# Optimization experiments

Measured on AMD Instinct MI355X. Metric: run time of the kernel, lower is better.

The kernel has to match this reference:

```python
import jax, jax.numpy as jnp
import numpy as np

N_VARS = 4000
N_LITS = 2 * N_VARS
N_CLAUSES = 16000
N_CELLS = 48000
DIM = 128
N_ROUNDS = 16
N_PROBS = 8


def _mlp(x, w1, b1, w2, b2, w3, b3):
    x = jax.nn.relu(x @ w1.T + b1)
    x = jax.nn.relu(x @ w2.T + b2)
    return x @ w3.T + b3


def _lstm_step(x, h, c, wih, whh, bih, bhh):
    # PyTorch LSTM gate order: i, f, g, o
    gates = x @ wih.T + bih + h @ whh.T + bhh
    i, f, g, o = jnp.split(gates, 4, axis=-1)
    c = jax.nn.sigmoid(f) * c + jax.nn.sigmoid(i) * jnp.tanh(g)
    h = jax.nn.sigmoid(o) * jnp.tanh(c)
    return h, c


def setup_inputs() -> dict:
    key = jax.random.key(0)
    ks = iter(jax.random.split(key, 64))

    def p(shape, scale=0.05):
        return jax.random.normal(next(ks), shape, dtype=jnp.float32) * scale

    lit_idx = jax.random.randint(next(ks), (N_CELLS,), 0, N_LITS)
    cls_idx = jax.random.randint(next(ks), (N_CELLS,), 0, N_CLAUSES)
    L_unpack_indices = jnp.stack([lit_idx, cls_idx], axis=1)  # [n_cells, 2]

    return dict(
        L_unpack_indices=L_unpack_indices,
        n_vars=N_VARS, n_probs=N_PROBS, n_rounds=N_ROUNDS,
        L_init_w=p((DIM, 1)), L_init_b=p((DIM,)),
        C_init_w=p((DIM, 1)), C_init_b=p((DIM,)),
        Lmsg_w1=p((DIM, DIM)), Lmsg_b1=p((DIM,)),
        Lmsg_w2=p((DIM, DIM)), Lmsg_b2=p((DIM,)),
        Lmsg_w3=p((DIM, DIM)), Lmsg_b3=p((DIM,)),
        Cmsg_w1=p((DIM, DIM)), Cmsg_b1=p((DIM,)),
        Cmsg_w2=p((DIM, DIM)), Cmsg_b2=p((DIM,)),
        Cmsg_w3=p((DIM, DIM)), Cmsg_b3=p((DIM,)),
        Lvote_w1=p((DIM, DIM)), Lvote_b1=p((DIM,)),
        Lvote_w2=p((DIM, DIM)), Lvote_b2=p((DIM,)),
        Lvote_w3=p((1, DIM)), Lvote_b3=p((1,)),
        Lu_wih=p((4 * DIM, 2 * DIM)), Lu_whh=p((4 * DIM, DIM)),
        Lu_bih=p((4 * DIM,)), Lu_bhh=p((4 * DIM,)),
        Cu_wih=p((4 * DIM, DIM)), Cu_whh=p((4 * DIM, DIM)),
        Cu_bih=p((4 * DIM,)), Cu_bhh=p((4 * DIM,)),
    )


def reference(L_unpack_indices, n_vars, n_probs, n_rounds,
              L_init_w, L_init_b, C_init_w, C_init_b,
              Lmsg_w1, Lmsg_b1, Lmsg_w2, Lmsg_b2, Lmsg_w3, Lmsg_b3,
              Cmsg_w1, Cmsg_b1, Cmsg_w2, Cmsg_b2, Cmsg_w3, Cmsg_b3,
              Lvote_w1, Lvote_b1, Lvote_w2, Lvote_b2, Lvote_w3, Lvote_b3,
              Lu_wih, Lu_whh, Lu_bih, Lu_bhh,
              Cu_wih, Cu_whh, Cu_bih, Cu_bhh):
    n_lits = 2 * n_vars
    dim = L_init_b.shape[0]
    n_clauses = N_CLAUSES

    # densified literal-clause incidence matrix (matches torch.sparse -> to_dense)
    M = jnp.zeros((n_lits, n_clauses), jnp.float32).at[
        L_unpack_indices[:, 0], L_unpack_indices[:, 1]].add(1.0)

    # L_init/C_init applied to ts = ones(1)
    L0 = jnp.broadcast_to(L_init_w[:, 0] + L_init_b, (n_lits, dim))
    C0 = jnp.broadcast_to(C_init_w[:, 0] + C_init_b, (n_clauses, dim))
    carry0 = (L0, jnp.zeros((n_lits, dim), jnp.float32),
              C0, jnp.zeros((n_clauses, dim), jnp.float32))

    def round_fn(carry, _):
        Lh, Lc, Ch, Cc = carry
        L_pre = _mlp(Lh, Lmsg_w1, Lmsg_b1, Lmsg_w2, Lmsg_b2, Lmsg_w3, Lmsg_b3)
        LC_msg = M.T @ L_pre                      # [n_clauses, dim]
        Ch, Cc = _lstm_step(LC_msg, Ch, Cc, Cu_wih, Cu_whh, Cu_bih, Cu_bhh)
        C_pre = _mlp(Ch, Cmsg_w1, Cmsg_b1, Cmsg_w2, Cmsg_b2, Cmsg_w3, Cmsg_b3)
        CL_msg = M @ C_pre                        # [n_lits, dim]
        flipped = jnp.concatenate([Lh[n_vars:2 * n_vars], Lh[:n_vars]], axis=0)
        Lh, Lc = _lstm_step(jnp.concatenate([CL_msg, flipped], axis=1),
                            Lh, Lc, Lu_wih, Lu_whh, Lu_bih, Lu_bhh)
        return (Lh, Lc, Ch, Cc), None

    (Lh, _, _, _), _ = jax.lax.scan(round_fn, carry0, None, length=n_rounds)

    vote = _mlp(Lh, Lvote_w1, Lvote_b1, Lvote_w2, Lvote_b2, Lvote_w3, Lvote_b3)  # [n_lits, 1]
    vote_join = jnp.concatenate([vote[:n_vars], vote[n_vars:]], axis=1)          # [n_vars, 2]
    vote_join = vote_join.reshape(n_probs, -1)
    return jnp.mean(vote_join, axis=1)
```

## Files before the change

### kernel.cpp

```cpp
#include <hip/hip_runtime.h>
#include <cstdint>
#include <cstddef>

#define N_VARS   4000
#define N_LITS   8000
#define N_CLAUSES 16000
#define N_CELLS  48000
#define DIM      128
#define N_ROUNDS 16
#define N_PROBS  8

typedef __bf16 bf16x8 __attribute__((ext_vector_type(8)));
typedef float f32x4 __attribute__((ext_vector_type(4)));

__device__ inline unsigned short f2bf(float x) {
  unsigned int u = __float_as_uint(x);
  u += 0x7fffu + ((u >> 16) & 1u);
  return (unsigned short)(u >> 16);
}
__device__ inline float bflo(unsigned int v) { return __uint_as_float(v << 16); }
__device__ inline float bfhi(unsigned int v) { return __uint_as_float(v & 0xffff0000u); }
__device__ inline unsigned int pack2(float a, float b) {
  return (unsigned int)f2bf(a) | ((unsigned int)f2bf(b) << 16);
}
__device__ inline bf16x8 ld_frag(const unsigned short* p) {
  uint4 u = *reinterpret_cast<const uint4*>(p);
  return __builtin_bit_cast(bf16x8, u);
}
__device__ inline float fast_sigmoid(float x) { return 1.f / (1.f + __expf(-x)); }
__device__ inline float fast_tanh(float x) {
  float t = __expf(-2.f * x);
  return (1.f - t) / (1.f + t);
}


template<int KS, bool LIT>
__global__ __launch_bounds__(512, 4) void fused_round(
    const int* __restrict__ ptr, const int* __restrict__ col,
    const unsigned short* __restrict__ Tsrc,
    const unsigned short* hold, unsigned short* hnew,
    float* __restrict__ cst,
    const unsigned short* __restrict__ Wp, const float* __restrict__ bP,
    const unsigned short* __restrict__ Wm1, const float* __restrict__ bm1,
    const unsigned short* __restrict__ Wm2, const float* __restrict__ bm2,
    const unsigned short* __restrict__ Wm3, const float* __restrict__ bm3,
    unsigned short* __restrict__ Tout) {
  __shared__ __align__(16) unsigned short msg[32][136];
  __shared__ __align__(16) unsigned short hsA[32][136];
  __shared__ __align__(16) unsigned short hsF[LIT ? 32 : 1][136];
  __shared__ __align__(16) unsigned short xb[32][136];
  const int tid = threadIdx.x;
  const int w = tid >> 6, l = tid & 63;
  const int r = l & 15, kc = l >> 4;
  const int row0 = blockIdx.x * 32;
  const int flipoff = LIT ? ((row0 < N_VARS) ? N_VARS : -N_VARS) : 0;

  float s[16];
  {
    const int g8 = tid >> 3, gl = tid & 7;
    const int grow = g8 & 31, part = g8 >> 5;
    const int row = row0 + grow;
    const int b = ptr[row], e = ptr[row + 1];
#pragma unroll
    for (int q = 0; q < 16; ++q) s[q] = 0.f;
    int j = b + part;
    int c0 = (j < e) ? col[j] : 0;
    while (j < e) {
      const int jn = j + 2;
      const int c1 = (jn < e) ? col[jn] : 0;
      const unsigned short* src = &Tsrc[(size_t)c0 * 128 + gl * 16];
      const uint4 v0 = *reinterpret_cast<const uint4*>(src);
      const uint4 v1 = *reinterpret_cast<const uint4*>(src + 8);
      s[0]  += bflo(v0.x); s[1]  += bfhi(v0.x);
      s[2]  += bflo(v0.y); s[3]  += bfhi(v0.y);
      s[4]  += bflo(v0.z); s[5]  += bfhi(v0.z);
      s[6]  += bflo(v0.w); s[7]  += bfhi(v0.w);
      s[8]  += bflo(v1.x); s[9]  += bfhi(v1.x);
      s[10] += bflo(v1.y); s[11] += bfhi(v1.y);
      s[12] += bflo(v1.z); s[13] += bfhi(v1.z);
      s[14] += bflo(v1.w); s[15] += bfhi(v1.w);
      j = jn; c0 = c1;
    }
    if (part == 1) {
      uint4 o0, o1;
      o0.x = pack2(s[0], s[1]);  o0.y = pack2(s[2], s[3]);
      o0.z = pack2(s[4], s[5]);  o0.w = pack2(s[6], s[7]);
      o1.x = pack2(s[8], s[9]);  o1.y = pack2(s[10], s[11]);
      o1.z = pack2(s[12], s[13]); o1.w = pack2(s[14], s[15]);
      *reinterpret_cast<uint4*>(&msg[grow][gl * 16]) = o0;
      *reinterpret_cast<uint4*>(&msg[grow][gl * 16 + 8]) = o1;
    }
  }
  __syncthreads();

  {
    const int g8 = tid >> 3, gl = tid & 7;
    const int grow = g8 & 31, part = g8 >> 5;
    if (part == 0) {
      const uint4 m0 = *reinterpret_cast<const uint4*>(&msg[grow][gl * 16]);
      const uint4 m1 = *reinterpret_cast<const uint4*>(&msg[grow][gl * 16 + 8]);
      s[0]  += bflo(m0.x); s[1]  += bfhi(m0.x);
      s[2]  += bflo(m0.y); s[3]  += bfhi(m0.y);
      s[4]  += bflo(m0.z); s[5]  += bfhi(m0.z);
      s[6]  += bflo(m0.w); s[7]  += bfhi(m0.w);
      s[8]  += bflo(m1.x); s[9]  += bfhi(m1.x);
      s[10] += bflo(m1.y); s[11] += bfhi(m1.y);
      s[12] += bflo(m1.z); s[13] += bfhi(m1.z);
      s[14] += bflo(m1.w); s[15] += bfhi(m1.w);
      uint4 o0, o1;
      o0.x = pack2(s[0], s[1]);  o0.y = pack2(s[2], s[3]);
      o0.z = pack2(s[4], s[5]);  o0.w = pack2(s[6], s[7]);
      o1.x = pack2(s[8], s[9]);  o1.y = pack2(s[10], s[11]);
      o1.z = pack2(s[12], s[13]); o1.w = pack2(s[14], s[15]);
      *reinterpret_cast<uint4*>(&msg[grow][gl * 16]) = o0;
      *reinterpret_cast<uint4*>(&msg[grow][gl * 16 + 8]) = o1;
    } else {
      const int sidx = tid - 256;
#pragma unroll
      for (int q = 0; q < 2; ++q) {
        const int n = sidx + q * 256;
        const int rw = n >> 4, c8 = (n & 15) * 8;
        *reinterpret_cast<uint4*>(&hsA[rw][c8]) =
            *reinterpret_cast<const uint4*>(&hold[(size_t)(row0 + rw) * 128 + c8]);
        if (LIT)
          *reinterpret_cast<uint4*>(&hsF[rw][c8]) =
              *reinterpret_cast<const uint4*>(&hold[(size_t)(row0 + flipoff + rw) * 128 + c8]);
      }
    }
  }
  __syncthreads();

  f32x4 acc[2][4];
#pragma unroll
  for (int rg = 0; rg < 2; ++rg)
#pragma unroll
    for (int t = 0; t < 4; ++t) acc[rg][t] = (f32x4){0.f, 0.f, 0.f, 0.f};

#pragma unroll
  for (int ks = 0; ks < KS; ++ks) {
    bf16x8 bfr[2];
#pragma unroll
    for (int rg = 0; rg < 2; ++rg) {
      const int xr = rg * 16 + r;
      if (ks < 4)        bfr[rg] = ld_frag(&msg[xr][ks * 32 + kc * 8]);
      else if (!LIT)     bfr[rg] = ld_frag(&hsA[xr][(ks - 4) * 32 + kc * 8]);
      else if (ks < 8)   bfr[rg] = ld_frag(&hsF[xr][(ks - 4) * 32 + kc * 8]);
      else               bfr[rg] = ld_frag(&hsA[xr][(ks - 8) * 32 + kc * 8]);
    }
#pragma unroll
    for (int tt = 0; tt < 4; ++tt) {
      bf16x8 afr = ld_frag(&Wp[(size_t)(((w * KS + ks) * 4 + tt) * 64 + l) * 8]);
      acc[0][tt] = __builtin_amdgcn_mfma_f32_16x16x32_bf16(afr, bfr[0], acc[0][tt], 0, 0, 0);
      acc[1][tt] = __builtin_amdgcn_mfma_f32_16x16x32_bf16(afr, bfr[1], acc[1][tt], 0, 0, 0);
    }
  }
  __syncthreads();

  {
    const int d0 = w * 16 + kc * 4;
#pragma unroll
    for (int rg = 0; rg < 2; ++rg) {
      const int row = row0 + rg * 16 + r;
      const size_t cb = (size_t)row * 128 + d0;
      f32x4 cv = *reinterpret_cast<const f32x4*>(&cst[cb]);
      f32x4 cn4;
      unsigned int hp[2];
#pragma unroll
      for (int tt = 0; tt < 4; ++tt) {
        const float4 bb = *reinterpret_cast<const float4*>(&bP[w * 64 + tt * 16 + kc * 4]);
        float ig = acc[rg][tt][0] + bb.x;
        float fg = acc[rg][tt][1] + bb.y;
        float gg = acc[rg][tt][2] + bb.z;
        float og = acc[rg][tt][3] + bb.w;
        float cn = fast_sigmoid(fg) * cv[tt] + fast_sigmoid(ig) * fast_tanh(gg);
        float hv = fast_sigmoid(og) * fast_tanh(cn);
        cn4[tt] = cn;
        if (tt & 1) hp[tt >> 1] |= (unsigned int)f2bf(hv) << 16;
        else        hp[tt >> 1]  = (unsigned int)f2bf(hv);
      }
      *reinterpret_cast<f32x4*>(&cst[cb]) = cn4;
      uint2 hv2 = {hp[0], hp[1]};
      *reinterpret_cast<uint2*>(&hnew[cb]) = hv2;
      *reinterpret_cast<uint2*>(&hsA[rg * 16 + r][d0]) = hv2;
    }
  }
  __syncthreads();

  const int mrg = w >> 2;
  const int t0 = (w & 3) * 2;
  {
    f32x4 a2[2] = {(f32x4){0.f, 0.f, 0.f, 0.f}, (f32x4){0.f, 0.f, 0.f, 0.f}};
#pragma unroll
    for (int ks = 0; ks < 4; ++ks) {
      bf16x8 af = ld_frag(&hsA[mrg * 16 + r][ks * 32 + kc * 8]);
#pragma unroll
      for (int q = 0; q < 2; ++q) {
        bf16x8 bf = ld_frag(&Wm1[(size_t)(((t0 + q) * 4 + ks) * 64 + l) * 8]);
        a2[q] = __builtin_amdgcn_mfma_f32_16x16x32_bf16(af, bf, a2[q], 0, 0, 0);
      }
    }
#pragma unroll
    for (int q = 0; q < 2; ++q) {
      float bv = bm1[(t0 + q) * 16 + r];
#pragma unroll
      for (int j = 0; j < 4; ++j)
        xb[mrg * 16 + kc * 4 + j][(t0 + q) * 16 + r] = f2bf(fmaxf(a2[q][j] + bv, 0.f));
    }
  }
  __syncthreads();
  {
    f32x4 a2[2] = {(f32x4){0.f, 0.f, 0.f, 0.f}, (f32x4){0.f, 0.f, 0.f, 0.f}};
#pragma unroll
    for (int ks = 0; ks < 4; ++ks) {
      bf16x8 af = ld_frag(&xb[mrg * 16 + r][ks * 32 + kc * 8]);
#pragma unroll
      for (int q = 0; q < 2; ++q) {
        bf16x8 bf = ld_frag(&Wm2[(size_t)(((t0 + q) * 4 + ks) * 64 + l) * 8]);
        a2[q] = __builtin_amdgcn_mfma_f32_16x16x32_bf16(af, bf, a2[q], 0, 0, 0);
      }
    }
#pragma unroll
    for (int q = 0; q < 2; ++q) {
      float bv = bm2[(t0 + q) * 16 + r];
#pragma unroll
      for (int j = 0; j < 4; ++j)
        msg[mrg * 16 + kc * 4 + j][(t0 + q) * 16 + r] = f2bf(fmaxf(a2[q][j] + bv, 0.f));
    }
  }
  __syncthreads();
  {
    f32x4 a2[2] = {(f32x4){0.f, 0.f, 0.f, 0.f}, (f32x4){0.f, 0.f, 0.f, 0.f}};
#pragma unroll
    for (int ks = 0; ks < 4; ++ks) {
      bf16x8 af = ld_frag(&msg[mrg * 16 + r][ks * 32 + kc * 8]);
#pragma unroll
      for (int q = 0; q < 2; ++q) {
        bf16x8 bf = ld_frag(&Wm3[(size_t)(((t0 + q) * 4 + ks) * 64 + l) * 8]);
        a2[q] = __builtin_amdgcn_mfma_f32_16x16x32_bf16(af, bf, a2[q], 0, 0, 0);
      }
    }
#pragma unroll
    for (int q = 0; q < 2; ++q) {
      float bv = bm3[(t0 + q) * 16 + r];
#pragma unroll
      for (int j = 0; j < 4; ++j)
        Tout[(size_t)(row0 + mrg * 16 + kc * 4 + j) * 128 + (t0 + q) * 16 + r] =
            f2bf(a2[q][j] + bv);
    }
  }
}

__global__ __launch_bounds__(256) void fused_mlp3(
    const unsigned short* __restrict__ A,
    const unsigned short* __restrict__ W1, const float* __restrict__ b1,
    const unsigned short* __restrict__ W2, const float* __restrict__ b2,
    const unsigned short* __restrict__ W3, const float* __restrict__ b3,
    unsigned short* __restrict__ out) {
  __shared__ __align__(16) unsigned short xbuf[2][4][16][136];
  const int w = threadIdx.x >> 6, l = threadIdx.x & 63;
  const int r = l & 15, kc = l >> 4;
  const int row0 = blockIdx.x * 64 + w * 16;

  f32x4 acc[8];
#pragma unroll
  for (int t = 0; t < 8; ++t) acc[t] = (f32x4){0.f, 0.f, 0.f, 0.f};
#pragma unroll
  for (int ks = 0; ks < 4; ++ks) {
    bf16x8 a = ld_frag(&A[(size_t)(row0 + r) * 128 + ks * 32 + kc * 8]);
#pragma unroll
    for (int t = 0; t < 8; ++t) {
      bf16x8 b = ld_frag(&W1[(size_t)((t * 4 + ks) * 64 + l) * 8]);
      acc[t] = __builtin_amdgcn_mfma_f32_16x16x32_bf16(a, b, acc[t], 0, 0, 0);
    }
  }
#pragma unroll
  for (int t = 0; t < 8; ++t) {
    float bv = b1[t * 16 + r];
#pragma unroll
    for (int j = 0; j < 4; ++j)
      xbuf[0][w][kc * 4 + j][t * 16 + r] = f2bf(fmaxf(acc[t][j] + bv, 0.f));
  }
#pragma unroll
  for (int t = 0; t < 8; ++t) acc[t] = (f32x4){0.f, 0.f, 0.f, 0.f};
#pragma unroll
  for (int ks = 0; ks < 4; ++ks) {
    bf16x8 a = ld_frag(&xbuf[0][w][r][ks * 32 + kc * 8]);
#pragma unroll
    for (int t = 0; t < 8; ++t) {
      bf16x8 b = ld_frag(&W2[(size_t)((t * 4 + ks) * 64 + l) * 8]);
      acc[t] = __builtin_amdgcn_mfma_f32_16x16x32_bf16(a, b, acc[t], 0, 0, 0);
    }
  }
#pragma unroll
  for (int t = 0; t < 8; ++t) {
    float bv = b2[t * 16 + r];
#pragma unroll
    for (int j = 0; j < 4; ++j)
      xbuf[1][w][kc * 4 + j][t * 16 + r] = f2bf(fmaxf(acc[t][j] + bv, 0.f));
  }
#pragma unroll
  for (int t = 0; t < 8; ++t) acc[t] = (f32x4){0.f, 0.f, 0.f, 0.f};
#pragma unroll
  for (int ks = 0; ks < 4; ++ks) {
    bf16x8 a = ld_frag(&xbuf[1][w][r][ks * 32 + kc * 8]);
#pragma unroll
    for (int t = 0; t < 8; ++t) {
      bf16x8 b = ld_frag(&W3[(size_t)((t * 4 + ks) * 64 + l) * 8]);
      acc[t] = __builtin_amdgcn_mfma_f32_16x16x32_bf16(a, b, acc[t], 0, 0, 0);
    }
  }
#pragma unroll
  for (int t = 0; t < 8; ++t) {
    float bv = b3[t * 16 + r];
#pragma unroll
    for (int j = 0; j < 4; ++j)
      out[(size_t)(row0 + kc * 4 + j) * 128 + t * 16 + r] = f2bf(acc[t][j] + bv);
  }
}

__global__ __launch_bounds__(256) void fused_vote(
    const unsigned short* __restrict__ A,
    const unsigned short* __restrict__ W1, const float* __restrict__ b1,
    const unsigned short* __restrict__ W2, const float* __restrict__ b2,
    const float* __restrict__ w3, const float* __restrict__ b3,
    float* __restrict__ vote) {
  __shared__ __align__(16) unsigned short xbuf[4][16][136];
  const int w = threadIdx.x >> 6, l = threadIdx.x & 63;
  const int r = l & 15, kc = l >> 4;
  const int row0 = blockIdx.x * 64 + w * 16;

  f32x4 acc[8];
#pragma unroll
  for (int t = 0; t < 8; ++t) acc[t] = (f32x4){0.f, 0.f, 0.f, 0.f};
#pragma unroll
  for (int ks = 0; ks < 4; ++ks) {
    bf16x8 a = ld_frag(&A[(size_t)(row0 + r) * 128 + ks * 32 + kc * 8]);
#pragma unroll
    for (int t = 0; t < 8; ++t) {
      bf16x8 b = ld_frag(&W1[(size_t)((t * 4 + ks) * 64 + l) * 8]);
      acc[t] = __builtin_amdgcn_mfma_f32_16x16x32_bf16(a, b, acc[t], 0, 0, 0);
    }
  }
#pragma unroll
  for (int t = 0; t < 8; ++t) {
    float bv = b1[t * 16 + r];
#pragma unroll
    for (int j = 0; j < 4; ++j)
      xbuf[w][kc * 4 + j][t * 16 + r] = f2bf(fmaxf(acc[t][j] + bv, 0.f));
  }
#pragma unroll
  for (int t = 0; t < 8; ++t) acc[t] = (f32x4){0.f, 0.f, 0.f, 0.f};
#pragma unroll
  for (int ks = 0; ks < 4; ++ks) {
    bf16x8 a = ld_frag(&xbuf[w][r][ks * 32 + kc * 8]);
#pragma unroll
    for (int t = 0; t < 8; ++t) {
      bf16x8 b = ld_frag(&W2[(size_t)((t * 4 + ks) * 64 + l) * 8]);
      acc[t] = __builtin_amdgcn_mfma_f32_16x16x32_bf16(a, b, acc[t], 0, 0, 0);
    }
  }
  float vs[4] = {0.f, 0.f, 0.f, 0.f};
#pragma unroll
  for (int t = 0; t < 8; ++t) {
    float bv = b2[t * 16 + r], wv = w3[t * 16 + r];
#pragma unroll
    for (int j = 0; j < 4; ++j)
      vs[j] += fmaxf(acc[t][j] + bv, 0.f) * wv;
  }
#pragma unroll
  for (int off = 1; off < 16; off <<= 1) {
#pragma unroll
    for (int j = 0; j < 4; ++j) vs[j] += __shfl_xor(vs[j], off, 16);
  }
  if (r == 0) {
#pragma unroll
    for (int j = 0; j < 4; ++j) vote[row0 + kc * 4 + j] = vs[j] + b3[0];
  }
}

__global__ void init_state_kernel(const float* __restrict__ Lw, const float* __restrict__ Lb,
                                  const float* __restrict__ Cw, const float* __restrict__ Cb,
                                  unsigned short* __restrict__ Lh, float* __restrict__ Lc,
                                  unsigned short* __restrict__ Ch, float* __restrict__ Cc) {
  int idx = blockIdx.x * 256 + threadIdx.x;
  if (idx >= N_CLAUSES * DIM) return;
  int d = idx & 127;
  Ch[idx] = f2bf(Cw[d] + Cb[d]);
  Cc[idx] = 0.f;
  if (idx < N_LITS * DIM) {
    Lh[idx] = f2bf(Lw[d] + Lb[d]);
    Lc[idx] = 0.f;
  }
}

__global__ void pack8_kernel(const float* s0, const float* s1, const float* s2, const float* s3,
                             const float* s4, const float* s5, const float* s6, const float* s7,
                             unsigned short* d0, unsigned short* d1, unsigned short* d2,
                             unsigned short* d3, unsigned short* d4, unsigned short* d5,
                             unsigned short* d6, unsigned short* d7) {
  int i = blockIdx.x * 256 + threadIdx.x;
  const float* s; unsigned short* d;
  switch (blockIdx.y) {
    case 0: s = s0; d = d0; break;
    case 1: s = s1; d = d1; break;
    case 2: s = s2; d = d2; break;
    case 3: s = s3; d = d3; break;
    case 4: s = s4; d = d4; break;
    case 5: s = s5; d = d5; break;
    case 6: s = s6; d = d6; break;
    default: s = s7; d = d7; break;
  }
  int np = i >> 7, k = i & 127;
  int tt = np >> 4, r = np & 15;
  int ks = k >> 5, kcf = (k >> 3) & 3, e = k & 7;
  int dst = (((tt * 4 + ks) * 64) + kcf * 16 + r) * 8 + e;
  d[dst] = f2bf(s[i]);
}

template<int KIH>
__global__ void pack_gates_kernel(const float* __restrict__ wih, const float* __restrict__ whh,
                                  const float* __restrict__ bih, const float* __restrict__ bhh,
                                  unsigned short* __restrict__ Wp, float* __restrict__ bP) {
  constexpr int K = KIH + 128;
  constexpr int KS = K / 32;
  int idx = blockIdx.x * 256 + threadIdx.x;
  if (idx >= 512 * K) return;
  int np = idx / K, k = idx % K;
  int gt = np & 3;
  int d = ((np >> 6) << 4) + (((np >> 2) & 3) << 2) + ((np >> 4) & 3);
  int orig = gt * 128 + d;
  float v = (k < KIH) ? wih[(size_t)orig * KIH + k] : whh[(size_t)orig * 128 + (k - KIH)];
  int w = np >> 6, tt = (np >> 4) & 3, r = np & 15;
  int ks = k >> 5, kcf = (k >> 3) & 3, e = k & 7;
  size_t dst = ((size_t)((w * KS + ks) * 4 + tt) * 64 + kcf * 16 + r) * 8 + e;
  Wp[dst] = f2bf(v);
  if (k == 0) bP[np] = bih[orig] + bhh[orig];
}

__global__ void count_kernel(const int* __restrict__ uidx,
                             int* __restrict__ lit_cnt, int* __restrict__ cls_cnt) {
  int i = blockIdx.x * 256 + threadIdx.x;
  if (i < N_CELLS) {
    atomicAdd(&lit_cnt[uidx[2 * i]], 1);
    atomicAdd(&cls_cnt[uidx[2 * i + 1]], 1);
  }
}

__global__ void scan_kernel(const int* __restrict__ cnt, int* __restrict__ ptr, int n) {
  __shared__ int part[1024];
  __shared__ int total;
  int t = threadIdx.x;
  int chunk = (n + 1023) >> 10;
  int lo = t * chunk, hi = min(lo + chunk, n);
  int s = 0;
  for (int i = lo; i < hi; ++i) s += cnt[i];
  part[t] = s;
  __syncthreads();
  if (t == 0) {
    int acc = 0;
    for (int i = 0; i < 1024; ++i) { int v = part[i]; part[i] = acc; acc += v; }
    total = acc;
  }
  __syncthreads();
  int acc = part[t];
  for (int i = lo; i < hi; ++i) { ptr[i] = acc; acc += cnt[i]; }
  if (t == 0) ptr[n] = total;
}

__global__ void scatter_kernel(const int* __restrict__ uidx,
                               const int* __restrict__ lit_ptr, const int* __restrict__ cls_ptr,
                               int* __restrict__ lit_fill, int* __restrict__ cls_fill,
                               int* __restrict__ lit_col, int* __restrict__ cls_col) {
  int i = blockIdx.x * 256 + threadIdx.x;
  if (i < N_CELLS) {
    int lit = uidx[2 * i], cls = uidx[2 * i + 1];
    int p = atomicAdd(&lit_fill[lit], 1);
    lit_col[lit_ptr[lit] + p] = cls;
    int q = atomicAdd(&cls_fill[cls], 1);
    cls_col[cls_ptr[cls] + q] = lit;
  }
}

__global__ void prob_mean_kernel(const float* __restrict__ vote, float* __restrict__ out) {
  int p = blockIdx.x;
  int t = threadIdx.x;
  float s = 0.f;
  for (int i = t; i < 500; i += 256) s += vote[p * 500 + i] + vote[N_VARS + p * 500 + i];
  __shared__ float red[256];
  red[t] = s;
  __syncthreads();
  for (int off = 128; off > 0; off >>= 1) {
    if (t < off) red[t] += red[t + off];
    __syncthreads();
  }
  if (t == 0) out[p] = red[0] * (1.0f / 1000.0f);
}

extern "C" void kernel_launch(void* const* d_in, const int* in_sizes, int n_in,
                              void* d_out, int out_size, void* d_ws, size_t ws_size,
                              hipStream_t stream) {
  (void)in_sizes; (void)n_in; (void)out_size;
  const int* uidx = (const int*)d_in[0];
  const float* L_init_w = (const float*)d_in[4];
  const float* L_init_b = (const float*)d_in[5];
  const float* C_init_w = (const float*)d_in[6];
  const float* C_init_b = (const float*)d_in[7];
  const float* Lmsg_w1 = (const float*)d_in[8],  *Lmsg_b1 = (const float*)d_in[9];
  const float* Lmsg_w2 = (const float*)d_in[10], *Lmsg_b2 = (const float*)d_in[11];
  const float* Lmsg_w3 = (const float*)d_in[12], *Lmsg_b3 = (const float*)d_in[13];
  const float* Cmsg_w1 = (const float*)d_in[14], *Cmsg_b1 = (const float*)d_in[15];
  const float* Cmsg_w2 = (const float*)d_in[16], *Cmsg_b2 = (const float*)d_in[17];
  const float* Cmsg_w3 = (const float*)d_in[18], *Cmsg_b3 = (const float*)d_in[19];
  const float* Lvote_w1 = (const float*)d_in[20], *Lvote_b1 = (const float*)d_in[21];
  const float* Lvote_w2 = (const float*)d_in[22], *Lvote_b2 = (const float*)d_in[23];
  const float* Lvote_w3 = (const float*)d_in[24], *Lvote_b3 = (const float*)d_in[25];
  const float* Lu_wih = (const float*)d_in[26], *Lu_whh = (const float*)d_in[27];
  const float* Lu_bih = (const float*)d_in[28], *Lu_bhh = (const float*)d_in[29];
  const float* Cu_wih = (const float*)d_in[30], *Cu_whh = (const float*)d_in[31];
  const float* Cu_bih = (const float*)d_in[32], *Cu_bhh = (const float*)d_in[33];
  float* out = (float*)d_out;

  char* base = (char*)d_ws;
  size_t off = 0;
  auto alloc = [&](size_t bytes) {
    void* p = base + off;
    off = (off + bytes + 255) & ~(size_t)255;
    return p;
  };
  float* Lc   = (float*)alloc((size_t)N_LITS * DIM * 4);
  float* Cc   = (float*)alloc((size_t)N_CLAUSES * DIM * 4);
  float* bL   = (float*)alloc(512 * 4);
  float* bC   = (float*)alloc(512 * 4);
  float* vote = (float*)alloc(N_LITS * 4);
  unsigned short* LhA = (unsigned short*)alloc((size_t)N_LITS * DIM * 2);
  unsigned short* LhB = (unsigned short*)alloc((size_t)N_LITS * DIM * 2);
  unsigned short* Ch  = (unsigned short*)alloc((size_t)N_CLAUSES * DIM * 2);
  unsigned short* TL  = (unsigned short*)alloc((size_t)N_LITS * DIM * 2);
  unsigned short* TC  = (unsigned short*)alloc((size_t)N_CLAUSES * DIM * 2);
  unsigned short* WLp = (unsigned short*)alloc(512 * 384 * 2);
  unsigned short* WCp = (unsigned short*)alloc(512 * 256 * 2);
  unsigned short* wLm1 = (unsigned short*)alloc(DIM * DIM * 2);
  unsigned short* wLm2 = (unsigned short*)alloc(DIM * DIM * 2);
  unsigned short* wLm3 = (unsigned short*)alloc(DIM * DIM * 2);
  unsigned short* wCm1 = (unsigned short*)alloc(DIM * DIM * 2);
  unsigned short* wCm2 = (unsigned short*)alloc(DIM * DIM * 2);
  unsigned short* wCm3 = (unsigned short*)alloc(DIM * DIM * 2);
  unsigned short* wV1  = (unsigned short*)alloc(DIM * DIM * 2);
  unsigned short* wV2  = (unsigned short*)alloc(DIM * DIM * 2);
  int* lit_cnt  = (int*)alloc(N_LITS * 4);
  int* cls_cnt  = (int*)alloc(N_CLAUSES * 4);
  int* lit_fill = (int*)alloc(N_LITS * 4);
  int* cls_fill = (int*)alloc(N_CLAUSES * 4);
  int* lit_ptr  = (int*)alloc((N_LITS + 1) * 4);
  int* cls_ptr  = (int*)alloc((N_CLAUSES + 1) * 4);
  int* lit_col  = (int*)alloc(N_CELLS * 4);
  int* cls_col  = (int*)alloc(N_CELLS * 4);
  if (off > ws_size) return;

  hipMemsetAsync(lit_cnt, 0, (char*)lit_ptr - (char*)lit_cnt, stream);
  count_kernel<<<(N_CELLS + 255) / 256, 256, 0, stream>>>(uidx, lit_cnt, cls_cnt);
  scan_kernel<<<1, 1024, 0, stream>>>(lit_cnt, lit_ptr, N_LITS);
  scan_kernel<<<1, 1024, 0, stream>>>(cls_cnt, cls_ptr, N_CLAUSES);
  scatter_kernel<<<(N_CELLS + 255) / 256, 256, 0, stream>>>(
      uidx, lit_ptr, cls_ptr, lit_fill, cls_fill, lit_col, cls_col);

  init_state_kernel<<<(N_CLAUSES * DIM + 255) / 256, 256, 0, stream>>>(
      L_init_w, L_init_b, C_init_w, C_init_b, LhA, Lc, Ch, Cc);
  pack_gates_kernel<256><<<(512 * 384 + 255) / 256, 256, 0, stream>>>(
      Lu_wih, Lu_whh, Lu_bih, Lu_bhh, WLp, bL);
  pack_gates_kernel<128><<<(512 * 256 + 255) / 256, 256, 0, stream>>>(
      Cu_wih, Cu_whh, Cu_bih, Cu_bhh, WCp, bC);
  dim3 cgrid(DIM * DIM / 256, 8);
  pack8_kernel<<<cgrid, 256, 0, stream>>>(
      Lmsg_w1, Lmsg_w2, Lmsg_w3, Cmsg_w1, Cmsg_w2, Cmsg_w3, Lvote_w1, Lvote_w2,
      wLm1, wLm2, wLm3, wCm1, wCm2, wCm3, wV1, wV2);

  fused_mlp3<<<N_LITS / 64, 256, 0, stream>>>(
      LhA, wLm1, Lmsg_b1, wLm2, Lmsg_b2, wLm3, Lmsg_b3, TL);

  for (int r = 0; r < N_ROUNDS; ++r) {
    fused_round<8, false><<<N_CLAUSES / 32, 512, 0, stream>>>(
        cls_ptr, cls_col, TL, Ch, Ch, Cc, WCp, bC,
        wCm1, Cmsg_b1, wCm2, Cmsg_b2, wCm3, Cmsg_b3, TC);
    const unsigned short* lold = (r & 1) ? LhB : LhA;
    unsigned short* lnew = (r & 1) ? LhA : LhB;
    fused_round<12, true><<<N_LITS / 32, 512, 0, stream>>>(
        lit_ptr, lit_col, TC, lold, lnew, Lc, WLp, bL,
        wLm1, Lmsg_b1, wLm2, Lmsg_b2, wLm3, Lmsg_b3, TL);
  }

  fused_vote<<<N_LITS / 64, 256, 0, stream>>>(
      LhA, wV1, Lvote_b1, wV2, Lvote_b2, Lvote_w3, Lvote_b3, vote);
  prob_mean_kernel<<<N_PROBS, 256, 0, stream>>>(vote, out);
}
```

Baseline: 715.7 us.

## Double rows per block in fused round kernel to reuse weight fragments

Each fused_round block now handles 64 rows instead of 32, so every weight fragment loaded from global memory feeds four MFMA row groups instead of two, halving weight traffic per row. The MLP stages are remapped so each wave owns one 16-column output slice across all 64 rows. The flip buffer now aliases xb, with an extra barrier added before xb and msg are overwritten, and the launch-bounds occupancy hint is dropped. The cost is more registers and LDS per block and half as many blocks (125 for the literal pass), which lowers parallelism on a large GPU.

```diff
diff --git a/kernel.cpp b/kernel.cpp
--- a/kernel.cpp
+++ b/kernel.cpp
@@ -35,7 +35,7 @@
 
 
 template<int KS, bool LIT>
-__global__ __launch_bounds__(512, 4) void fused_round(
+__global__ __launch_bounds__(512) void fused_round(
     const int* __restrict__ ptr, const int* __restrict__ col,
     const unsigned short* __restrict__ Tsrc,
     const unsigned short* hold, unsigned short* hnew,
@@ -45,102 +45,97 @@
     const unsigned short* __restrict__ Wm2, const float* __restrict__ bm2,
     const unsigned short* __restrict__ Wm3, const float* __restrict__ bm3,
     unsigned short* __restrict__ Tout) {
-  __shared__ __align__(16) unsigned short msg[32][136];
-  __shared__ __align__(16) unsigned short hsA[32][136];
-  __shared__ __align__(16) unsigned short hsF[LIT ? 32 : 1][136];
-  __shared__ __align__(16) unsigned short xb[32][136];
+  __shared__ __align__(16) unsigned short msg[64][136];
+  __shared__ __align__(16) unsigned short hsA[64][136];
+  __shared__ __align__(16) unsigned short xb[64][136];
+  auto hsF = xb;
   const int tid = threadIdx.x;
   const int w = tid >> 6, l = tid & 63;
   const int r = l & 15, kc = l >> 4;
-  const int row0 = blockIdx.x * 32;
-  const int flipoff = LIT ? ((row0 < N_VARS) ? N_VARS : -N_VARS) : 0;
-
-  float s[16];
+  const int row0 = blockIdx.x * 64;
+
+  float s[32];
   {
-    const int g8 = tid >> 3, gl = tid & 7;
-    const int grow = g8 & 31, part = g8 >> 5;
+    const int g4 = tid >> 2, gl = tid & 3;
+    const int grow = g4 & 63, part = g4 >> 6;
     const int row = row0 + grow;
     const int b = ptr[row], e = ptr[row + 1];
 #pragma unroll
-    for (int q = 0; q < 16; ++q) s[q] = 0.f;
+    for (int q = 0; q < 32; ++q) s[q] = 0.f;
     int j = b + part;
     int c0 = (j < e) ? col[j] : 0;
     while (j < e) {
       const int jn = j + 2;
       const int c1 = (jn < e) ? col[jn] : 0;
-      const unsigned short* src = &Tsrc[(size_t)c0 * 128 + gl * 16];
-      const uint4 v0 = *reinterpret_cast<const uint4*>(src);
-      const uint4 v1 = *reinterpret_cast<const uint4*>(src + 8);
-      s[0]  += bflo(v0.x); s[1]  += bfhi(v0.x);
-      s[2]  += bflo(v0.y); s[3]  += bfhi(v0.y);
-      s[4]  += bflo(v0.z); s[5]  += bfhi(v0.z);
-      s[6]  += bflo(v0.w); s[7]  += bfhi(v0.w);
-      s[8]  += bflo(v1.x); s[9]  += bfhi(v1.x);
-      s[10] += bflo(v1.y); s[11] += bfhi(v1.y);
-      s[12] += bflo(v1.z); s[13] += bfhi(v1.z);
-      s[14] += bflo(v1.w); s[15] += bfhi(v1.w);
+      const unsigned short* src = &Tsrc[(size_t)c0 * 128 + gl * 32];
+#pragma unroll
+      for (int q = 0; q < 4; ++q) {
+        const uint4 v = *reinterpret_cast<const uint4*>(src + q * 8);
+        s[q * 8 + 0] += bflo(v.x); s[q * 8 + 1] += bfhi(v.x);
+        s[q * 8 + 2] += bflo(v.y); s[q * 8 + 3] += bfhi(v.y);
+        s[q * 8 + 4] += bflo(v.z); s[q * 8 + 5] += bfhi(v.z);
+        s[q * 8 + 6] += bflo(v.w); s[q * 8 + 7] += bfhi(v.w);
+      }
       j = jn; c0 = c1;
     }
     if (part == 1) {
-      uint4 o0, o1;
-      o0.x = pack2(s[0], s[1]);  o0.y = pack2(s[2], s[3]);
-      o0.z = pack2(s[4], s[5]);  o0.w = pack2(s[6], s[7]);
-      o1.x = pack2(s[8], s[9]);  o1.y = pack2(s[10], s[11]);
-      o1.z = pack2(s[12], s[13]); o1.w = pack2(s[14], s[15]);
-      *reinterpret_cast<uint4*>(&msg[grow][gl * 16]) = o0;
-      *reinterpret_cast<uint4*>(&msg[grow][gl * 16 + 8]) = o1;
+#pragma unroll
+      for (int q = 0; q < 4; ++q) {
+        uint4 o;
+        o.x = pack2(s[q * 8 + 0], s[q * 8 + 1]);
+        o.y = pack2(s[q * 8 + 2], s[q * 8 + 3]);
+        o.z = pack2(s[q * 8 + 4], s[q * 8 + 5]);
+        o.w = pack2(s[q * 8 + 6], s[q * 8 + 7]);
+        *reinterpret_cast<uint4*>(&msg[grow][gl * 32 + q * 8]) = o;
+      }
     }
   }
   __syncthreads();
 
   {
-    const int g8 = tid >> 3, gl = tid & 7;
-    const int grow = g8 & 31, part = g8 >> 5;
+    const int g4 = tid >> 2, gl = tid & 3;
+    const int grow = g4 & 63, part = g4 >> 6;
     if (part == 0) {
-      const uint4 m0 = *reinterpret_cast<const uint4*>(&msg[grow][gl * 16]);
-      const uint4 m1 = *reinterpret_cast<const uint4*>(&msg[grow][gl * 16 + 8]);
-      s[0]  += bflo(m0.x); s[1]  += bfhi(m0.x);
-      s[2]  += bflo(m0.y); s[3]  += bfhi(m0.y);
-      s[4]  += bflo(m0.z); s[5]  += bfhi(m0.z);
-      s[6]  += bflo(m0.w); s[7]  += bfhi(m0.w);
-      s[8]  += bflo(m1.x); s[9]  += bfhi(m1.x);
-      s[10] += bflo(m1.y); s[11] += bfhi(m1.y);
-      s[12] += bflo(m1.z); s[13] += bfhi(m1.z);
-      s[14] += bflo(m1.w); s[15] += bfhi(m1.w);
-      uint4 o0, o1;
-      o0.x = pack2(s[0], s[1]);  o0.y = pack2(s[2], s[3]);
-      o0.z = pack2(s[4], s[5]);  o0.w = pack2(s[6], s[7]);
-      o1.x = pack2(s[8], s[9]);  o1.y = pack2(s[10], s[11]);
-      o1.z = pack2(s[12], s[13]); o1.w = pack2(s[14], s[15]);
-      *reinterpret_cast<uint4*>(&msg[grow][gl * 16]) = o0;
-      *reinterpret_cast<uint4*>(&msg[grow][gl * 16 + 8]) = o1;
+#pragma unroll
+      for (int q = 0; q < 4; ++q) {
+        const uint4 m = *reinterpret_cast<const uint4*>(&msg[grow][gl * 32 + q * 8]);
+        uint4 o;
+        o.x = pack2(s[q * 8 + 0] + bflo(m.x), s[q * 8 + 1] + bfhi(m.x));
+        o.y = pack2(s[q * 8 + 2] + bflo(m.y), s[q * 8 + 3] + bfhi(m.y));
+        o.z = pack2(s[q * 8 + 4] + bflo(m.z), s[q * 8 + 5] + bfhi(m.z));
+        o.w = pack2(s[q * 8 + 6] + bflo(m.w), s[q * 8 + 7] + bfhi(m.w));
+        *reinterpret_cast<uint4*>(&msg[grow][gl * 32 + q * 8]) = o;
+      }
     } else {
       const int sidx = tid - 256;
 #pragma unroll
-      for (int q = 0; q < 2; ++q) {
+      for (int q = 0; q < 4; ++q) {
         const int n = sidx + q * 256;
         const int rw = n >> 4, c8 = (n & 15) * 8;
         *reinterpret_cast<uint4*>(&hsA[rw][c8]) =
             *reinterpret_cast<const uint4*>(&hold[(size_t)(row0 + rw) * 128 + c8]);
-        if (LIT)
+        if (LIT) {
+          const int grow2 = row0 + rw;
+          const int fr = (grow2 < N_VARS) ? grow2 + N_VARS : grow2 - N_VARS;
           *reinterpret_cast<uint4*>(&hsF[rw][c8]) =
-              *reinterpret_cast<const uint4*>(&hold[(size_t)(row0 + flipoff + rw) * 128 + c8]);
-      }
-    }
-  }
-  __syncthreads();
-
-  f32x4 acc[2][4];
-#pragma unroll
-  for (int rg = 0; rg < 2; ++rg)
+              *reinterpret_cast<const uint4*>(&hold[(size_t)fr * 128 + c8]);
+        }
+      }
+    }
+  }
+  __syncthreads();
+
+  f32x4 acc[4][4];
+#pragma unroll
+  for (int rg = 0; rg < 4; ++rg)
 #pragma unroll
     for (int t = 0; t < 4; ++t) acc[rg][t] = (f32x4){0.f, 0.f, 0.f, 0.f};
 
 #pragma unroll
   for (int ks = 0; ks < KS; ++ks) {
-    bf16x8 bfr[2];
-#pragma unroll
-    for (int rg = 0; rg < 2; ++rg) {
+    bf16x8 bfr[4];
+#pragma unroll
+    for (int rg = 0; rg < 4; ++rg) {
       const int xr = rg * 16 + r;
       if (ks < 4)        bfr[rg] = ld_frag(&msg[xr][ks * 32 + kc * 8]);
       else if (!LIT)     bfr[rg] = ld_frag(&hsA[xr][(ks - 4) * 32 + kc * 8]);
@@ -150,8 +145,9 @@
 #pragma unroll
     for (int tt = 0; tt < 4; ++tt) {
       bf16x8 afr = ld_frag(&Wp[(size_t)(((w * KS + ks) * 4 + tt) * 64 + l) * 8]);
-      acc[0][tt] = __builtin_amdgcn_mfma_f32_16x16x32_bf16(afr, bfr[0], acc[0][tt], 0, 0, 0);
-      acc[1][tt] = __builtin_amdgcn_mfma_f32_16x16x32_bf16(afr, bfr[1], acc[1][tt], 0, 0, 0);
+#pragma unroll
+      for (int rg = 0; rg < 4; ++rg)
+        acc[rg][tt] = __builtin_amdgcn_mfma_f32_16x16x32_bf16(afr, bfr[rg], acc[rg][tt], 0, 0, 0);
     }
   }
   __syncthreads();
@@ -159,7 +155,7 @@
   {
     const int d0 = w * 16 + kc * 4;
 #pragma unroll
-    for (int rg = 0; rg < 2; ++rg) {
+    for (int rg = 0; rg < 4; ++rg) {
       const int row = row0 + rg * 16 + r;
       const size_t cb = (size_t)row * 128 + d0;
       f32x4 cv = *reinterpret_cast<const f32x4*>(&cst[cb]);
@@ -186,67 +182,70 @@
   }
   __syncthreads();
 
-  const int mrg = w >> 2;
-  const int t0 = (w & 3) * 2;
   {
-    f32x4 a2[2] = {(f32x4){0.f, 0.f, 0.f, 0.f}, (f32x4){0.f, 0.f, 0.f, 0.f}};
+    f32x4 a2[4];
+#pragma unroll
+    for (int rg = 0; rg < 4; ++rg) a2[rg] = (f32x4){0.f, 0.f, 0.f, 0.f};
 #pragma unroll
     for (int ks = 0; ks < 4; ++ks) {
-      bf16x8 af = ld_frag(&hsA[mrg * 16 + r][ks * 32 + kc * 8]);
-#pragma unroll
-      for (int q = 0; q < 2; ++q) {
-        bf16x8 bf = ld_frag(&Wm1[(size_t)(((t0 + q) * 4 + ks) * 64 + l) * 8]);
-        a2[q] = __builtin_amdgcn_mfma_f32_16x16x32_bf16(af, bf, a2[q], 0, 0, 0);
-      }
-    }
-#pragma unroll
-    for (int q = 0; q < 2; ++q) {
-      float bv = bm1[(t0 + q) * 16 + r];
+      bf16x8 wf = ld_frag(&Wm1[(size_t)((w * 4 + ks) * 64 + l) * 8]);
+#pragma unroll
+      for (int rg = 0; rg < 4; ++rg) {
+        bf16x8 af = ld_frag(&hsA[rg * 16 + r][ks * 32 + kc * 8]);
+        a2[rg] = __builtin_amdgcn_mfma_f32_16x16x32_bf16(af, wf, a2[rg], 0, 0, 0);
+      }
+    }
+    float bv = bm1[w * 16 + r];
+    __syncthreads();
+#pragma unroll
+    for (int rg = 0; rg < 4; ++rg)
 #pragma unroll
       for (int j = 0; j < 4; ++j)
-        xb[mrg * 16 + kc * 4 + j][(t0 + q) * 16 + r] = f2bf(fmaxf(a2[q][j] + bv, 0.f));
-    }
+        xb[rg * 16 + kc * 4 + j][w * 16 + r] = f2bf(fmaxf(a2[rg][j] + bv, 0.f));
   }
   __syncthreads();
   {
-    f32x4 a2[2] = {(f32x4){0.f, 0.f, 0.f, 0.f}, (f32x4){0.f, 0.f, 0.f, 0.f}};
+    f32x4 a2[4];
+#pragma unroll
+    for (int rg = 0; rg < 4; ++rg) a2[rg] = (f32x4){0.f, 0.f, 0.f, 0.f};
 #pragma unroll
     for (int ks = 0; ks < 4; ++ks) {
-      bf16x8 af = ld_frag(&xb[mrg * 16 + r][ks * 32 + kc * 8]);
-#pragma unroll
-      for (int q = 0; q < 2; ++q) {
-        bf16x8 bf = ld_frag(&Wm2[(size_t)(((t0 + q) * 4 + ks) * 64 + l) * 8]);
-        a2[q] = __builtin_amdgcn_mfma_f32_16x16x32_bf16(af, bf, a2[q], 0, 0, 0);
-      }
-    }
-#pragma unroll
-    for (int q = 0; q < 2; ++q) {
-      float bv = bm2[(t0 + q) * 16 + r];
+      bf16x8 wf = ld_frag(&Wm2[(size_t)((w * 4 + ks) * 64 + l) * 8]);
+#pragma unroll
+      for (int rg = 0; rg < 4; ++rg) {
+        bf16x8 af = ld_frag(&xb[rg * 16 + r][ks * 32 + kc * 8]);
+        a2[rg] = __builtin_amdgcn_mfma_f32_16x16x32_bf16(af, wf, a2[rg], 0, 0, 0);
+      }
+    }
+    float bv = bm2[w * 16 + r];
+    __syncthreads();
+#pragma unroll
+    for (int rg = 0; rg < 4; ++rg)
 #pragma unroll
       for (int j = 0; j < 4; ++j)
-        msg[mrg * 16 + kc * 4 + j][(t0 + q) * 16 + r] = f2bf(fmaxf(a2[q][j] + bv, 0.f));
-    }
+        msg[rg * 16 + kc * 4 + j][w * 16 + r] = f2bf(fmaxf(a2[rg][j] + bv, 0.f));
   }
   __syncthreads();
   {
-    f32x4 a2[2] = {(f32x4){0.f, 0.f, 0.f, 0.f}, (f32x4){0.f, 0.f, 0.f, 0.f}};
+    f32x4 a2[4];
+#pragma unroll
+    for (int rg = 0; rg < 4; ++rg) a2[rg] = (f32x4){0.f, 0.f, 0.f, 0.f};
 #pragma unroll
     for (int ks = 0; ks < 4; ++ks) {
-      bf16x8 af = ld_frag(&msg[mrg * 16 + r][ks * 32 + kc * 8]);
-#pragma unroll
-      for (int q = 0; q < 2; ++q) {
-        bf16x8 bf = ld_frag(&Wm3[(size_t)(((t0 + q) * 4 + ks) * 64 + l) * 8]);
-        a2[q] = __builtin_amdgcn_mfma_f32_16x16x32_bf16(af, bf, a2[q], 0, 0, 0);
-      }
-    }
-#pragma unroll
-    for (int q = 0; q < 2; ++q) {
-      float bv = bm3[(t0 + q) * 16 + r];
+      bf16x8 wf = ld_frag(&Wm3[(size_t)((w * 4 + ks) * 64 + l) * 8]);
+#pragma unroll
+      for (int rg = 0; rg < 4; ++rg) {
+        bf16x8 af = ld_frag(&msg[rg * 16 + r][ks * 32 + kc * 8]);
+        a2[rg] = __builtin_amdgcn_mfma_f32_16x16x32_bf16(af, wf, a2[rg], 0, 0, 0);
+      }
+    }
+    float bv = bm3[w * 16 + r];
+#pragma unroll
+    for (int rg = 0; rg < 4; ++rg)
 #pragma unroll
       for (int j = 0; j < 4; ++j)
-        Tout[(size_t)(row0 + mrg * 16 + kc * 4 + j) * 128 + (t0 + q) * 16 + r] =
-            f2bf(a2[q][j] + bv);
-    }
+        Tout[(size_t)(row0 + rg * 16 + kc * 4 + j) * 128 + w * 16 + r] =
+            f2bf(a2[rg][j] + bv);
   }
 }
 
@@ -579,12 +578,12 @@
       LhA, wLm1, Lmsg_b1, wLm2, Lmsg_b2, wLm3, Lmsg_b3, TL);
 
   for (int r = 0; r < N_ROUNDS; ++r) {
-    fused_round<8, false><<<N_CLAUSES / 32, 512, 0, stream>>>(
+    fused_round<8, false><<<N_CLAUSES / 64, 512, 0, stream>>>(
         cls_ptr, cls_col, TL, Ch, Ch, Cc, WCp, bC,
         wCm1, Cmsg_b1, wCm2, Cmsg_b2, wCm3, Cmsg_b3, TC);
     const unsigned short* lold = (r & 1) ? LhB : LhA;
     unsigned short* lnew = (r & 1) ? LhA : LhB;
-    fused_round<12, true><<<N_LITS / 32, 512, 0, stream>>>(
+    fused_round<12, true><<<N_LITS / 64, 512, 0, stream>>>(
         lit_ptr, lit_col, TC, lold, lnew, Lc, WLp, bL,
         wLm1, Lmsg_b1, wLm2, Lmsg_b2, wLm3, Lmsg_b3, TL);
   }
```

After: 961.9 us. 1.34x slower.

## Prefetch weight fragments and hidden-state tiles, swizzle shared-memory rows

Applied to the files above, without the earlier changes.

The fused round kernel now issues global loads for the previous hidden-state tiles and the first weight fragments before the sparse gather, double-buffers the LSTM weight fragments across the k-loop, and prefetches the first MLP layer weights before the barrier. All shared-memory tiles use an XOR swizzle on the column index keyed by the row. The aim is to hide global load latency behind the gather and MFMA work and to cut LDS bank conflicts. In exchange, register pressure rises, which may hurt occupancy under the 512x4 launch bounds, and the padded rows combined with the swizzle may not reduce conflicts further.

```diff
diff --git a/kernel.cpp b/kernel.cpp
--- a/kernel.cpp
+++ b/kernel.cpp
@@ -32,6 +32,7 @@
   float t = __expf(-2.f * x);
   return (1.f - t) / (1.f + t);
 }
+__device__ inline int swz(int row, int si) { return si ^ ((row & 7) << 3); }
 
 
 template<int KS, bool LIT>
@@ -53,7 +54,27 @@
   const int w = tid >> 6, l = tid & 63;
   const int r = l & 15, kc = l >> 4;
   const int row0 = blockIdx.x * 32;
-  const int flipoff = LIT ? ((row0 < N_VARS) ? N_VARS : -N_VARS) : 0;
+
+  bf16x8 wcur[4];
+#pragma unroll
+  for (int tt = 0; tt < 4; ++tt)
+    wcur[tt] = ld_frag(&Wp[(size_t)(((w * KS + 0) * 4 + tt) * 64 + l) * 8]);
+
+  uint4 stA[2], stF[2];
+  if (tid >= 256) {
+    const int sidx = tid - 256;
+#pragma unroll
+    for (int q = 0; q < 2; ++q) {
+      const int n = sidx + q * 256;
+      const int rw = n >> 4, c8 = (n & 15) * 8;
+      stA[q] = *reinterpret_cast<const uint4*>(&hold[(size_t)(row0 + rw) * 128 + c8]);
+      if (LIT) {
+        const int gr = row0 + rw;
+        const int fr = (gr < N_VARS) ? gr + N_VARS : gr - N_VARS;
+        stF[q] = *reinterpret_cast<const uint4*>(&hold[(size_t)fr * 128 + c8]);
+      }
+    }
+  }
 
   float s[16];
   {
@@ -87,8 +108,8 @@
       o0.z = pack2(s[4], s[5]);  o0.w = pack2(s[6], s[7]);
       o1.x = pack2(s[8], s[9]);  o1.y = pack2(s[10], s[11]);
       o1.z = pack2(s[12], s[13]); o1.w = pack2(s[14], s[15]);
-      *reinterpret_cast<uint4*>(&msg[grow][gl * 16]) = o0;
-      *reinterpret_cast<uint4*>(&msg[grow][gl * 16 + 8]) = o1;
+      *reinterpret_cast<uint4*>(&msg[grow][swz(grow, gl * 16)]) = o0;
+      *reinterpret_cast<uint4*>(&msg[grow][swz(grow, gl * 16 + 8)]) = o1;
     }
   }
   __syncthreads();
@@ -97,8 +118,8 @@
     const int g8 = tid >> 3, gl = tid & 7;
     const int grow = g8 & 31, part = g8 >> 5;
     if (part == 0) {
-      const uint4 m0 = *reinterpret_cast<const uint4*>(&msg[grow][gl * 16]);
-      const uint4 m1 = *reinterpret_cast<const uint4*>(&msg[grow][gl * 16 + 8]);
+      const uint4 m0 = *reinterpret_cast<const uint4*>(&msg[grow][swz(grow, gl * 16)]);
+      const uint4 m1 = *reinterpret_cast<const uint4*>(&msg[grow][swz(grow, gl * 16 + 8)]);
       s[0]  += bflo(m0.x); s[1]  += bfhi(m0.x);
       s[2]  += bflo(m0.y); s[3]  += bfhi(m0.y);
       s[4]  += bflo(m0.z); s[5]  += bfhi(m0.z);
@@ -112,19 +133,17 @@
       o0.z = pack2(s[4], s[5]);  o0.w = pack2(s[6], s[7]);
       o1.x = pack2(s[8], s[9]);  o1.y = pack2(s[10], s[11]);
       o1.z = pack2(s[12], s[13]); o1.w = pack2(s[14], s[15]);
-      *reinterpret_cast<uint4*>(&msg[grow][gl * 16]) = o0;
-      *reinterpret_cast<uint4*>(&msg[grow][gl * 16 + 8]) = o1;
+      *reinterpret_cast<uint4*>(&msg[grow][swz(grow, gl * 16)]) = o0;
+      *reinterpret_cast<uint4*>(&msg[grow][swz(grow, gl * 16 + 8)]) = o1;
     } else {
       const int sidx = tid - 256;
 #pragma unroll
       for (int q = 0; q < 2; ++q) {
         const int n = sidx + q * 256;
         const int rw = n >> 4, c8 = (n & 15) * 8;
-        *reinterpret_cast<uint4*>(&hsA[rw][c8]) =
-            *reinterpret_cast<const uint4*>(&hold[(size_t)(row0 + rw) * 128 + c8]);
+        *reinterpret_cast<uint4*>(&hsA[rw][swz(rw, c8)]) = stA[q];
         if (LIT)
-          *reinterpret_cast<uint4*>(&hsF[rw][c8]) =
-              *reinterpret_cast<const uint4*>(&hold[(size_t)(row0 + flipoff + rw) * 128 + c8]);
+          *reinterpret_cast<uint4*>(&hsF[rw][swz(rw, c8)]) = stF[q];
       }
     }
   }
@@ -138,22 +157,39 @@
 
 #pragma unroll
   for (int ks = 0; ks < KS; ++ks) {
+    bf16x8 wnext[4];
+    if (ks + 1 < KS) {
+#pragma unroll
+      for (int tt = 0; tt < 4; ++tt)
+        wnext[tt] = ld_frag(&Wp[(size_t)(((w * KS + ks + 1) * 4 + tt) * 64 + l) * 8]);
+    }
     bf16x8 bfr[2];
 #pragma unroll
     for (int rg = 0; rg < 2; ++rg) {
       const int xr = rg * 16 + r;
-      if (ks < 4)        bfr[rg] = ld_frag(&msg[xr][ks * 32 + kc * 8]);
-      else if (!LIT)     bfr[rg] = ld_frag(&hsA[xr][(ks - 4) * 32 + kc * 8]);
-      else if (ks < 8)   bfr[rg] = ld_frag(&hsF[xr][(ks - 4) * 32 + kc * 8]);
-      else               bfr[rg] = ld_frag(&hsA[xr][(ks - 8) * 32 + kc * 8]);
+      if (ks < 4)        bfr[rg] = ld_frag(&msg[xr][swz(xr, ks * 32 + kc * 8)]);
+      else if (!LIT)     bfr[rg] = ld_frag(&hsA[xr][swz(xr, (ks - 4) * 32 + kc * 8)]);
+      else if (ks < 8)   bfr[rg] = ld_frag(&hsF[xr][swz(xr, (ks - 4) * 32 + kc * 8)]);
+      else               bfr[rg] = ld_frag(&hsA[xr][swz(xr, (ks - 8) * 32 + kc * 8)]);
     }
 #pragma unroll
     for (int tt = 0; tt < 4; ++tt) {
-      bf16x8 afr = ld_frag(&Wp[(size_t)(((w * KS + ks) * 4 + tt) * 64 + l) * 8]);
-      acc[0][tt] = __builtin_amdgcn_mfma_f32_16x16x32_bf16(afr, bfr[0], acc[0][tt], 0, 0, 0);
-      acc[1][tt] = __builtin_amdgcn_mfma_f32_16x16x32_bf16(afr, bfr[1], acc[1][tt], 0, 0, 0);
-    }
-  }
+      acc[0][tt] = __builtin_amdgcn_mfma_f32_16x16x32_bf16(wcur[tt], bfr[0], acc[0][tt], 0, 0, 0);
+      acc[1][tt] = __builtin_amdgcn_mfma_f32_16x16x32_bf16(wcur[tt], bfr[1], acc[1][tt], 0, 0, 0);
+    }
+    if (ks + 1 < KS) {
+#pragma unroll
+      for (int tt = 0; tt < 4; ++tt) wcur[tt] = wnext[tt];
+    }
+  }
+
+  const int mrg = w >> 2;
+  const int t0 = (w & 3) * 2;
+  bf16x8 w1pre[2];
+#pragma unroll
+  for (int q = 0; q < 2; ++q)
+    w1pre[q] = ld_frag(&Wm1[(size_t)(((t0 + q) * 4 + 0) * 64 + l) * 8]);
+
   __syncthreads();
 
   {
@@ -181,21 +217,22 @@
       *reinterpret_cast<f32x4*>(&cst[cb]) = cn4;
       uint2 hv2 = {hp[0], hp[1]};
       *reinterpret_cast<uint2*>(&hnew[cb]) = hv2;
-      *reinterpret_cast<uint2*>(&hsA[rg * 16 + r][d0]) = hv2;
-    }
-  }
-  __syncthreads();
-
-  const int mrg = w >> 2;
-  const int t0 = (w & 3) * 2;
+      const int hr = rg * 16 + r;
+      *reinterpret_cast<uint2*>(&hsA[hr][swz(hr, d0)]) = hv2;
+    }
+  }
+  __syncthreads();
+
   {
     f32x4 a2[2] = {(f32x4){0.f, 0.f, 0.f, 0.f}, (f32x4){0.f, 0.f, 0.f, 0.f}};
 #pragma unroll
     for (int ks = 0; ks < 4; ++ks) {
-      bf16x8 af = ld_frag(&hsA[mrg * 16 + r][ks * 32 + kc * 8]);
+      const int ar = mrg * 16 + r;
+      bf16x8 af = ld_frag(&hsA[ar][swz(ar, ks * 32 + kc * 8)]);
 #pragma unroll
       for (int q = 0; q < 2; ++q) {
-        bf16x8 bf = ld_frag(&Wm1[(size_t)(((t0 + q) * 4 + ks) * 64 + l) * 8]);
+        bf16x8 bf = (ks == 0) ? w1pre[q]
+                  : ld_frag(&Wm1[(size_t)(((t0 + q) * 4 + ks) * 64 + l) * 8]);
         a2[q] = __builtin_amdgcn_mfma_f32_16x16x32_bf16(af, bf, a2[q], 0, 0, 0);
       }
     }
@@ -203,8 +240,10 @@
     for (int q = 0; q < 2; ++q) {
       float bv = bm1[(t0 + q) * 16 + r];
 #pragma unroll
-      for (int j = 0; j < 4; ++j)
-        xb[mrg * 16 + kc * 4 + j][(t0 + q) * 16 + r] = f2bf(fmaxf(a2[q][j] + bv, 0.f));
+      for (int j = 0; j < 4; ++j) {
+        const int orow = mrg * 16 + kc * 4 + j;
+        xb[orow][swz(orow, (t0 + q) * 16 + r)] = f2bf(fmaxf(a2[q][j] + bv, 0.f));
+      }
     }
   }
   __syncthreads();
@@ -212,7 +251,8 @@
     f32x4 a2[2] = {(f32x4){0.f, 0.f, 0.f, 0.f}, (f32x4){0.f, 0.f, 0.f, 0.f}};
 #pragma unroll
     for (int ks = 0; ks < 4; ++ks) {
-      bf16x8 af = ld_frag(&xb[mrg * 16 + r][ks * 32 + kc * 8]);
+      const int ar = mrg * 16 + r;
+      bf16x8 af = ld_frag(&xb[ar][swz(ar, ks * 32 + kc * 8)]);
 #pragma unroll
       for (int q = 0; q < 2; ++q) {
         bf16x8 bf = ld_frag(&Wm2[(size_t)(((t0 + q) * 4 + ks) * 64 + l) * 8]);
@@ -223,8 +263,10 @@
     for (int q = 0; q < 2; ++q) {
       float bv = bm2[(t0 + q) * 16 + r];
 #pragma unroll
-      for (int j = 0; j < 4; ++j)
-        msg[mrg * 16 + kc * 4 + j][(t0 + q) * 16 + r] = f2bf(fmaxf(a2[q][j] + bv, 0.f));
+      for (int j = 0; j < 4; ++j) {
+        const int orow = mrg * 16 + kc * 4 + j;
+        msg[orow][swz(orow, (t0 + q) * 16 + r)] = f2bf(fmaxf(a2[q][j] + bv, 0.f));
+      }
     }
   }
   __syncthreads();
@@ -232,7 +274,8 @@
     f32x4 a2[2] = {(f32x4){0.f, 0.f, 0.f, 0.f}, (f32x4){0.f, 0.f, 0.f, 0.f}};
 #pragma unroll
     for (int ks = 0; ks < 4; ++ks) {
-      bf16x8 af = ld_frag(&msg[mrg * 16 + r][ks * 32 + kc * 8]);
+      const int ar = mrg * 16 + r;
+      bf16x8 af = ld_frag(&msg[ar][swz(ar, ks * 32 + kc * 8)]);
 #pragma unroll
       for (int q = 0; q < 2; ++q) {
         bf16x8 bf = ld_frag(&Wm3[(size_t)(((t0 + q) * 4 + ks) * 64 + l) * 8]);
```

Measured after the change: 768.8 us. 1.07x slower.
